# Kernel tuning notes

Hardware: AMD Instinct MI355X
Metric: run time of the kernel (lower is better)

The kernel has to match this reference:

```python
import jax, jax.numpy as jnp
import numpy as np

HEAD_DIM = 128
NUM_HEADS = 16
GROUP_SIZE = 8


def setup_inputs() -> dict:
    key = jax.random.key(0)
    k1, k2, k3 = jax.random.split(key, 3)
    B, T, K = 2, 2048, 2048
    query = jax.random.normal(k1, (B, T, NUM_HEADS * HEAD_DIM), dtype=jnp.float32)
    k_ = jax.random.normal(k2, (B, K, NUM_HEADS, HEAD_DIM), dtype=jnp.float32)
    v_ = jax.random.normal(k3, (B, K, NUM_HEADS, HEAD_DIM), dtype=jnp.float32)
    return {"query": query, "key": k_, "value": v_}


def reference(query, key, value):
    B, T, _ = query.shape
    g = GROUP_SIZE
    # (B, T//g, g, H, D)
    gq = query.reshape(B, T // g, g, NUM_HEADS, HEAD_DIM)
    scale = jnp.sqrt(jnp.asarray(HEAD_DIM, dtype=query.dtype))
    # scores: (B, T//g, g, H, K)
    scores = jnp.einsum('btghd,bkhd->btghk', gq, key) / scale
    attention = jax.nn.softmax(scores, axis=-1)
    out = jnp.einsum('btghk,bkhd->btghd', attention, value)
    return out.reshape(B, T, -1)
```

## Files before the change

### kernel.cpp

```cpp
#include <hip/hip_runtime.h>


#define T_   2048
#define KLEN 2048
#define H_   16
#define D_   128
#define BH_  32
#define NT_  (KLEN / 64)

typedef unsigned short u16;
typedef short bf16x8 __attribute__((ext_vector_type(8), may_alias));
typedef float f32x4 __attribute__((ext_vector_type(4)));
typedef float f32x8 __attribute__((ext_vector_type(8), may_alias));
typedef float f32x16 __attribute__((ext_vector_type(16)));
typedef unsigned int u32a __attribute__((may_alias));
typedef u16 u16a __attribute__((may_alias));

__device__ __forceinline__ u16 f2bf(float f) {
    unsigned int u = __builtin_bit_cast(unsigned int, f);
    u += 0x7fffu + ((u >> 16) & 1u);
    return (u16)(u >> 16);
}
__device__ __forceinline__ unsigned int pk2(float a, float b) {
    unsigned int r;
    asm("v_cvt_pk_bf16_f32 %0, %1, %2" : "=v"(r) : "v"(a), "v"(b));
    return r;
}
__device__ __forceinline__ void pl_swap(unsigned int& a, unsigned int& b) {
    asm("v_permlane32_swap_b32 %0, %1" : "+v"(a), "+v"(b));
}

__device__ __forceinline__ void async_cp16(const void* g, void* l) {
    __builtin_amdgcn_global_load_lds(
        (const __attribute__((address_space(1))) unsigned int*)g,
        (__attribute__((address_space(3))) unsigned int*)l, 16, 0, 0);
}

#define FR_ELEMS ((size_t)KLEN * D_)
#define WS_NEED  (2 * BH_ * FR_ELEMS * sizeof(u16))
#define SM_BUF   32768

__global__ __launch_bounds__(256)
void prep_fused(const float* __restrict__ k_g, const float* __restrict__ v_g,
                u16* __restrict__ kf, u16* __restrict__ vf) {
    __shared__ __align__(16) unsigned char smk[16384];
    __shared__ __align__(16) unsigned char smv[16384];
    const int kt64 = blockIdx.x & 31;
    const int bh   = blockIdx.x >> 5;
    const int b = bh >> 4, h = bh & 15;
    const int tid = threadIdx.x;

    {
        const float* kbase = k_g + ((size_t)(b * KLEN + kt64 * 64) * H_ + h) * D_;
        #pragma unroll
        for (int i = 0; i < 4; ++i) {
            const int gid  = tid + 256 * i;
            const int row  = gid >> 4;
            const int col8 = gid & 15;
            f32x8 kv = *(const f32x8*)(kbase + (size_t)row * (H_ * D_) + col8 * 8);
            uint4 w;
            w.x = pk2(kv[0], kv[1]); w.y = pk2(kv[2], kv[3]);
            w.z = pk2(kv[4], kv[5]); w.w = pk2(kv[6], kv[7]);
            *(uint4*)(smk + row * 256 + ((col8 ^ (row & 15)) * 16)) = w;
        }
    }
    {
        const float* vbase = v_g + ((size_t)b * KLEN * H_ + h) * D_;
        const int sc0 = tid & 15;
        const int spr = tid >> 4;
        #pragma unroll
        for (int rr = 0; rr < 2; ++rr) {
            const int r0 = 2 * (spr + 16 * rr);
            const float* vp = vbase + (size_t)(kt64 * 64 + r0) * (H_ * D_) + sc0 * 8;
            f32x8 va = *(const f32x8*)vp;
            f32x8 vb = *(const f32x8*)(vp + H_ * D_);
            const int g_hi = r0 >> 3;
            const int woff = (r0 & 7) * 2;
            #pragma unroll
            for (int j = 0; j < 8; ++j) {
                const int d = sc0 * 8 + j;
                const int g = g_hi ^ ((d ^ (d >> 3)) & 7);
                *(u32a*)(smv + d * 128 + g * 16 + woff) = pk2(va[j], vb[j]);
            }
        }
    }
    __syncthreads();
    {
        u16* obase = kf + (size_t)bh * FR_ELEMS + (size_t)kt64 * 8192;
        #pragma unroll
        for (int i = 0; i < 4; ++i) {
            const int gid    = tid + 256 * i;
            const int lane   = gid & 63;
            const int dchunk = (gid >> 6) & 7;
            const int ktile  = gid >> 9;
            const int key  = ktile * 32 + (lane & 31);
            const int col8 = dchunk * 2 + (lane >> 5);
            uint4 w = *(const uint4*)(smk + key * 256 + ((col8 ^ (key & 15)) * 16));
            *(uint4*)(obase + (size_t)gid * 8) = w;
        }
    }
    {
        u16* obase = vf + (size_t)bh * FR_ELEMS;
        #pragma unroll
        for (int i = 0; i < 4; ++i) {
            const int gid   = tid + 256 * i;
            const int lane  = gid & 63;
            const int ntile = (gid >> 6) & 3;
            const int kc    = (gid >> 8) & 3;
            const int key0  = kc * 16 + (lane >> 5) * 8;
            const int d     = ntile * 32 + (lane & 31);
            const int g     = (key0 >> 3) ^ ((d ^ (d >> 3)) & 7);
            uint4 w = *(const uint4*)(smv + d * 128 + g * 16);
            *(uint4*)(obase + ((size_t)(kt64 * 16 + kc * 4 + ntile) * 64 + lane) * 8) = w;
        }
    }
}


struct PA2 { bf16x8 f0, f1; };

__device__ __forceinline__ PA2 softmax_pack(f32x16 st, float kexp, float& lacc) {
    float p[16];
    #pragma unroll
    for (int r = 0; r < 16; ++r) p[r] = exp2f(st[r] * kexp);
    lacc += (((p[0] + p[1]) + (p[2] + p[3])) + ((p[4] + p[5]) + (p[6] + p[7])))
          + (((p[8] + p[9]) + (p[10] + p[11])) + ((p[12] + p[13]) + (p[14] + p[15])));
    unsigned int a0 = pk2(p[0], p[1]),   b0 = pk2(p[4], p[5]);
    unsigned int a1 = pk2(p[2], p[3]),   b1 = pk2(p[6], p[7]);
    unsigned int a2 = pk2(p[8], p[9]),   b2 = pk2(p[12], p[13]);
    unsigned int a3 = pk2(p[10], p[11]), b3 = pk2(p[14], p[15]);
    pl_swap(a0, b0); pl_swap(a1, b1); pl_swap(a2, b2); pl_swap(a3, b3);
    uint4 w0; w0.x = a0; w0.y = a1; w0.z = b0; w0.w = b1;
    uint4 w1; w1.x = a2; w1.y = a3; w1.z = b2; w1.w = b3;
    PA2 r;
    r.f0 = __builtin_bit_cast(bf16x8, w0);
    r.f1 = __builtin_bit_cast(bf16x8, w1);
    return r;
}

__global__ __launch_bounds__(256, 1)
void gqa_fa7(const float* __restrict__ q_g, const u16* __restrict__ kf,
             const u16* __restrict__ vf, float* __restrict__ o_g) {
    __shared__ __align__(16) unsigned char smem[2 * SM_BUF];

    const int lane = threadIdx.x & 63;
    const int wave = threadIdx.x >> 6;
    const int half = lane >> 5;
    const int col  = lane & 31;

    const int blk = blockIdx.x;
    const int bh  = (blk & 7) * 4 + (blk >> 6);
    const int qt  = (blk >> 3) & 7;
    const int b = bh >> 4, h = bh & 15;

    const int q0 = qt * 256 + wave * 64;

    bf16x8 qfA[8], qfB[8];
    {
        const float* qbase = q_g + (size_t)(b * T_ + q0 + col) * (H_ * D_)
                                 + h * D_ + half * 8;
        #pragma unroll
        for (int dchunk = 0; dchunk < 8; ++dchunk) {
            f32x8 qv = *(const f32x8*)(qbase + dchunk * 16);
            uint4 w;
            w.x = pk2(qv[0], qv[1]); w.y = pk2(qv[2], qv[3]);
            w.z = pk2(qv[4], qv[5]); w.w = pk2(qv[6], qv[7]);
            qfA[dchunk] = __builtin_bit_cast(bf16x8, w);
        }
        const float* qbase2 = qbase + (size_t)32 * (H_ * D_);
        #pragma unroll
        for (int dchunk = 0; dchunk < 8; ++dchunk) {
            f32x8 qv = *(const f32x8*)(qbase2 + dchunk * 16);
            uint4 w;
            w.x = pk2(qv[0], qv[1]); w.y = pk2(qv[2], qv[3]);
            w.z = pk2(qv[4], qv[5]); w.w = pk2(qv[6], qv[7]);
            qfB[dchunk] = __builtin_bit_cast(bf16x8, w);
        }
    }

    const u16* KFb = kf + (size_t)bh * FR_ELEMS;
    const u16* VFb = vf + (size_t)bh * FR_ELEMS;

    f32x16 accA[4] = {}, accB[4] = {};
    float l_A = 0.f, l_B = 0.f;

    const float kexp = 0.12751744f;

    auto stage = [&](int buf, int kt) {
        const u16* ksrc = KFb + (size_t)kt * 8192;
        const u16* vsrc = VFb + (size_t)kt * 8192;
        unsigned char* base = smem + buf * SM_BUF;
        #pragma unroll
        for (int j = 0; j < 8; ++j) {
            const int idx = wave * 8 + j;
            if (idx < 16)
                async_cp16(ksrc + idx * 512 + lane * 8, base + idx * 1024);
            else
                async_cp16(vsrc + (idx - 16) * 512 + lane * 8,
                           base + 16384 + (idx - 16) * 1024);
        }
    };

    stage(0, 0);
    __syncthreads();

    for (int kt = 0; kt < NT_; ++kt) {
        const int cur = kt & 1;
        if (kt + 1 < NT_) stage(cur ^ 1, kt + 1);

        const unsigned char* kbuf = smem + cur * SM_BUF;
        const unsigned char* vbuf = kbuf + 16384;

        f32x16 sA0 = {}, sA1 = {}, sB0 = {}, sB1 = {};
        __builtin_amdgcn_s_setprio(1);
        #pragma unroll
        for (int dchunk = 0; dchunk < 8; ++dchunk) {
            bf16x8 kfr0 = *(const bf16x8*)(kbuf + dchunk * 1024 + lane * 16);
            bf16x8 kfr1 = *(const bf16x8*)(kbuf + (8 + dchunk) * 1024 + lane * 16);
            sA0 = __builtin_amdgcn_mfma_f32_32x32x16_bf16(kfr0, qfA[dchunk], sA0, 0, 0, 0);
            sA1 = __builtin_amdgcn_mfma_f32_32x32x16_bf16(kfr1, qfA[dchunk], sA1, 0, 0, 0);
            sB0 = __builtin_amdgcn_mfma_f32_32x32x16_bf16(kfr0, qfB[dchunk], sB0, 0, 0, 0);
            sB1 = __builtin_amdgcn_mfma_f32_32x32x16_bf16(kfr1, qfB[dchunk], sB1, 0, 0, 0);
        }
        __builtin_amdgcn_s_setprio(0);

        PA2 pA01 = softmax_pack(sA0, kexp, l_A);
        PA2 pA23 = softmax_pack(sA1, kexp, l_A);
        PA2 pB01 = softmax_pack(sB0, kexp, l_B);
        PA2 pB23 = softmax_pack(sB1, kexp, l_B);

        __builtin_amdgcn_s_setprio(1);
        #pragma unroll
        for (int kc = 0; kc < 4; ++kc) {
            const bf16x8 pa = (kc == 0) ? pA01.f0 : (kc == 1) ? pA01.f1
                            : (kc == 2) ? pA23.f0 : pA23.f1;
            const bf16x8 pb = (kc == 0) ? pB01.f0 : (kc == 1) ? pB01.f1
                            : (kc == 2) ? pB23.f0 : pB23.f1;
            #pragma unroll
            for (int nt2 = 0; nt2 < 4; ++nt2) {
                bf16x8 vfr = *(const bf16x8*)(vbuf + (kc * 4 + nt2) * 1024 + lane * 16);
                accA[nt2] = __builtin_amdgcn_mfma_f32_32x32x16_bf16(pa, vfr, accA[nt2], 0, 0, 0);
                accB[nt2] = __builtin_amdgcn_mfma_f32_32x32x16_bf16(pb, vfr, accB[nt2], 0, 0, 0);
            }
        }
        __builtin_amdgcn_s_setprio(0);

        __syncthreads();
    }

    const float lA_full = l_A + __shfl_xor(l_A, 32);
    const float lB_full = l_B + __shfl_xor(l_B, 32);
    float* lds_l = (float*)smem;
    if (half == 0) {
        lds_l[wave * 64 + col]      = 1.f / lA_full;
        lds_l[wave * 64 + 32 + col] = 1.f / lB_full;
    }
    __syncthreads();
    #pragma unroll
    for (int r = 0; r < 16; ++r) {
        const int qrow = (r & 3) + 8 * (r >> 2) + 4 * half;
        const float invA = lds_l[wave * 64 + qrow];
        const float invB = lds_l[wave * 64 + 32 + qrow];
        float* opA = o_g + (size_t)(b * T_ + q0 + qrow) * (H_ * D_) + h * D_ + col;
        float* opB = opA + (size_t)32 * (H_ * D_);
        #pragma unroll
        for (int nt2 = 0; nt2 < 4; ++nt2) {
            opA[nt2 * 32] = accA[nt2][r] * invA;
            opB[nt2 * 32] = accB[nt2][r] * invB;
        }
    }
}


#define VT_BYTES 16384
#define KT_BYTES (64 * 136 * 2)
#define PWF_BYTES 2304

__global__ __launch_bounds__(256, 2)
void gqa_fa_v1(const float* __restrict__ q_g, const float* __restrict__ k_g,
               const float* __restrict__ v_g, float* __restrict__ o_g) {
    __shared__ __align__(16) unsigned char smem[VT_BYTES + KT_BYTES + 4 * PWF_BYTES];
    unsigned char* VtB = smem;
    unsigned char* KtB = smem + VT_BYTES;
    const int lane = threadIdx.x & 63;
    const int wave = threadIdx.x >> 6;
    const int c    = lane & 15;
    const int quad = lane >> 4;
    const int qt = blockIdx.x & 31;
    const int bh = blockIdx.x >> 5;
    const int h  = bh & 15;
    const int b  = bh >> 4;
    const int q0 = qt * 64 + wave * 16;
    bf16x8 qf[4];
    {
        const float* qbase = q_g + (size_t)(b * T_ + q0 + c) * (H_ * D_) + h * D_ + quad * 8;
        #pragma unroll
        for (int dc = 0; dc < 4; ++dc) {
            f32x8 qv = *(const f32x8*)(qbase + dc * 32);
            uint4 w;
            w.x = pk2(qv[0], qv[1]); w.y = pk2(qv[2], qv[3]);
            w.z = pk2(qv[4], qv[5]); w.w = pk2(qv[6], qv[7]);
            qf[dc] = __builtin_bit_cast(bf16x8, w);
        }
    }
    f32x4 acc_o[8];
    #pragma unroll
    for (int dt = 0; dt < 8; ++dt) acc_o[dt] = (f32x4){0.f, 0.f, 0.f, 0.f};
    float m_i[4], l_i[4];
    #pragma unroll
    for (int r = 0; r < 4; ++r) { m_i[r] = -1e30f; l_i[r] = 0.f; }
    const float kexp = 0.12751744f;
    unsigned char* Pw = smem + VT_BYTES + KT_BYTES + wave * PWF_BYTES;
    const int sc0 = threadIdx.x & 15;
    const int spr = threadIdx.x >> 4;
    const size_t kvstride = (size_t)(H_ * D_);
    const float* kbase = k_g + ((size_t)b * KLEN * H_ + h) * D_;
    const float* vbase = v_g + ((size_t)b * KLEN * H_ + h) * D_;
    for (int kt = 0; kt < KLEN / 64; ++kt) {
        __syncthreads();
        #pragma unroll
        for (int i = 0; i < 4; ++i) {
            const int id   = threadIdx.x + 256 * i;
            const int row  = id >> 4;
            const int dcol = (id & 15) * 8;
            const float* kp = kbase + (size_t)(kt * 64 + row) * kvstride + dcol;
            f32x8 kv = *(const f32x8*)kp;
            uint4 w;
            w.x = pk2(kv[0], kv[1]); w.y = pk2(kv[2], kv[3]);
            w.z = pk2(kv[4], kv[5]); w.w = pk2(kv[6], kv[7]);
            *(uint4*)(KtB + (row * 136 + dcol) * 2) = w;
        }
        #pragma unroll
        for (int rr = 0; rr < 2; ++rr) {
            const int r0 = 2 * (spr + 16 * rr);
            const float* vp = vbase + (size_t)(kt * 64 + r0) * kvstride + sc0 * 8;
            f32x8 va = *(const f32x8*)vp;
            f32x8 vb = *(const f32x8*)(vp + kvstride);
            const int g_hi = r0 >> 3;
            const int woff = (r0 & 7) * 2;
            #pragma unroll
            for (int j = 0; j < 8; ++j) {
                const int d = sc0 * 8 + j;
                const int g = g_hi ^ ((d ^ (d >> 3)) & 7);
                *(u32a*)(VtB + d * 128 + g * 16 + woff) = pk2(va[j], vb[j]);
            }
        }
        __syncthreads();
        f32x4 s[4];
        #pragma unroll
        for (int nt = 0; nt < 4; ++nt) {
            s[nt] = (f32x4){0.f, 0.f, 0.f, 0.f};
            const u16* kfp = (const u16*)KtB + (nt * 16 + c) * 136 + quad * 8;
            #pragma unroll
            for (int dc = 0; dc < 4; ++dc) {
                bf16x8 kfr = *(const bf16x8*)(kfp + dc * 32);
                s[nt] = __builtin_amdgcn_mfma_f32_16x16x32_bf16(qf[dc], kfr, s[nt], 0, 0, 0);
            }
        }
        #pragma unroll
        for (int r = 0; r < 4; ++r) {
            float v = fmaxf(fmaxf(s[0][r], s[1][r]), fmaxf(s[2][r], s[3][r]));
            v = fmaxf(v, __shfl_xor(v, 1));
            v = fmaxf(v, __shfl_xor(v, 2));
            v = fmaxf(v, __shfl_xor(v, 4));
            v = fmaxf(v, __shfl_xor(v, 8));
            const float mnew  = fmaxf(m_i[r], v);
            const float alpha = exp2f((m_i[r] - mnew) * kexp);
            m_i[r] = mnew;
            l_i[r] *= alpha;
            #pragma unroll
            for (int dt = 0; dt < 8; ++dt) acc_o[dt][r] *= alpha;
            float sum = 0.f;
            #pragma unroll
            for (int nt = 0; nt < 4; ++nt) {
                const float p = exp2f((s[nt][r] - mnew) * kexp);
                sum += p;
                *(u16a*)(Pw + ((quad * 4 + r) * 72 + nt * 16 + c) * 2) = f2bf(p);
            }
            float t = sum;
            t += __shfl_xor(t, 1);
            t += __shfl_xor(t, 2);
            t += __shfl_xor(t, 4);
            t += __shfl_xor(t, 8);
            l_i[r] += t;
        }
        __syncthreads();
        #pragma unroll
        for (int kc = 0; kc < 2; ++kc) {
            bf16x8 pf = *(const bf16x8*)(Pw + (c * 72 + kc * 32 + quad * 8) * 2);
            const int k0 = kc * 32 + quad * 8;
            #pragma unroll
            for (int dt = 0; dt < 8; ++dt) {
                const int d = dt * 16 + c;
                const int g = (k0 >> 3) ^ ((d ^ (d >> 3)) & 7);
                bf16x8 vfr = *(const bf16x8*)(VtB + d * 128 + g * 16);
                acc_o[dt] = __builtin_amdgcn_mfma_f32_16x16x32_bf16(pf, vfr, acc_o[dt], 0, 0, 0);
            }
        }
    }
    #pragma unroll
    for (int r = 0; r < 4; ++r) {
        const float inv = 1.f / l_i[r];
        const int qrow = q0 + quad * 4 + r;
        float* op = o_g + (size_t)(b * T_ + qrow) * (H_ * D_) + h * D_ + c;
        #pragma unroll
        for (int dt = 0; dt < 8; ++dt)
            op[dt * 16] = acc_o[dt][r] * inv;
    }
}

extern "C" void kernel_launch(void* const* d_in, const int* in_sizes, int n_in,
                              void* d_out, int out_size, void* d_ws, size_t ws_size,
                              hipStream_t stream) {
    const float* q = (const float*)d_in[0];
    const float* k = (const float*)d_in[1];
    const float* v = (const float*)d_in[2];
    float* o = (float*)d_out;
    if (ws_size >= WS_NEED) {
        u16* kfb = (u16*)d_ws;
        u16* vfb = kfb + (size_t)BH_ * FR_ELEMS;
        prep_fused<<<dim3(1024), dim3(256), 0, stream>>>(k, v, kfb, vfb);
        gqa_fa7<<<dim3(256), dim3(256), 0, stream>>>(q, kfb, vfb, o);
    } else {
        gqa_fa_v1<<<dim3(1024), dim3(256), 0, stream>>>(q, k, v, o);
    }
}
```

Baseline: 237.9 us.

## Software-pipeline QK of next tile with softmax/PV of previous tile using triple buffering

Restructures the attention main loop so the QK^T MFMAs for tile kt are issued before the softmax and PV MFMAs for tile kt-1. LDS goes from double to triple buffering so the previous tile's V stays resident while the next tile loads. The aim is to overlap exp/softmax VALU work with matrix-core work and hide dependency latency. In exchange, registers held across iterations grow (an extra 64 floats of scores) and LDS use rises, which could cause spills.

```diff
diff --git a/kernel.cpp b/kernel.cpp
--- a/kernel.cpp
+++ b/kernel.cpp
@@ -139,9 +139,9 @@
 }
 
 __global__ __launch_bounds__(256, 1)
-void gqa_fa7(const float* __restrict__ q_g, const u16* __restrict__ kf,
+void gqa_fa9(const float* __restrict__ q_g, const u16* __restrict__ kf,
              const u16* __restrict__ vf, float* __restrict__ o_g) {
-    __shared__ __align__(16) unsigned char smem[2 * SM_BUF];
+    __shared__ __align__(16) unsigned char smem[3 * SM_BUF];
 
     const int lane = threadIdx.x & 63;
     const int wave = threadIdx.x >> 6;
@@ -201,34 +201,27 @@
         }
     };
 
-    stage(0, 0);
-    __syncthreads();
-
-    for (int kt = 0; kt < NT_; ++kt) {
-        const int cur = kt & 1;
-        if (kt + 1 < NT_) stage(cur ^ 1, kt + 1);
-
-        const unsigned char* kbuf = smem + cur * SM_BUF;
-        const unsigned char* vbuf = kbuf + 16384;
-
-        f32x16 sA0 = {}, sA1 = {}, sB0 = {}, sB1 = {};
+    auto qk_fused = [&](const unsigned char* kbuf, f32x16& dA0, f32x16& dA1,
+                        f32x16& dB0, f32x16& dB1) {
         __builtin_amdgcn_s_setprio(1);
         #pragma unroll
         for (int dchunk = 0; dchunk < 8; ++dchunk) {
             bf16x8 kfr0 = *(const bf16x8*)(kbuf + dchunk * 1024 + lane * 16);
             bf16x8 kfr1 = *(const bf16x8*)(kbuf + (8 + dchunk) * 1024 + lane * 16);
-            sA0 = __builtin_amdgcn_mfma_f32_32x32x16_bf16(kfr0, qfA[dchunk], sA0, 0, 0, 0);
-            sA1 = __builtin_amdgcn_mfma_f32_32x32x16_bf16(kfr1, qfA[dchunk], sA1, 0, 0, 0);
-            sB0 = __builtin_amdgcn_mfma_f32_32x32x16_bf16(kfr0, qfB[dchunk], sB0, 0, 0, 0);
-            sB1 = __builtin_amdgcn_mfma_f32_32x32x16_bf16(kfr1, qfB[dchunk], sB1, 0, 0, 0);
+            dA0 = __builtin_amdgcn_mfma_f32_32x32x16_bf16(kfr0, qfA[dchunk], dA0, 0, 0, 0);
+            dA1 = __builtin_amdgcn_mfma_f32_32x32x16_bf16(kfr1, qfA[dchunk], dA1, 0, 0, 0);
+            dB0 = __builtin_amdgcn_mfma_f32_32x32x16_bf16(kfr0, qfB[dchunk], dB0, 0, 0, 0);
+            dB1 = __builtin_amdgcn_mfma_f32_32x32x16_bf16(kfr1, qfB[dchunk], dB1, 0, 0, 0);
         }
         __builtin_amdgcn_s_setprio(0);
-
-        PA2 pA01 = softmax_pack(sA0, kexp, l_A);
-        PA2 pA23 = softmax_pack(sA1, kexp, l_A);
-        PA2 pB01 = softmax_pack(sB0, kexp, l_B);
-        PA2 pB23 = softmax_pack(sB1, kexp, l_B);
-
+    };
+
+    auto smpv_fused = [&](f32x16 tA0, f32x16 tA1, f32x16 tB0, f32x16 tB1,
+                          const unsigned char* vbuf) {
+        PA2 pA01 = softmax_pack(tA0, kexp, l_A);
+        PA2 pA23 = softmax_pack(tA1, kexp, l_A);
+        PA2 pB01 = softmax_pack(tB0, kexp, l_B);
+        PA2 pB23 = softmax_pack(tB1, kexp, l_B);
         __builtin_amdgcn_s_setprio(1);
         #pragma unroll
         for (int kc = 0; kc < 4; ++kc) {
@@ -244,9 +237,30 @@
             }
         }
         __builtin_amdgcn_s_setprio(0);
-
+    };
+
+    stage(0, 0);
+    __syncthreads();
+    stage(1, 1);
+    f32x16 psA0 = {}, psA1 = {}, psB0 = {}, psB1 = {};
+    qk_fused(smem, psA0, psA1, psB0, psB1);
+    __syncthreads();
+
+    int cur = 1, prev = 0;
+    for (int kt = 1; kt < NT_; ++kt) {
+        const int nxt = (cur == 2) ? 0 : cur + 1;
+        if (kt + 1 < NT_) stage(nxt, kt + 1);
+
+        f32x16 nsA0 = {}, nsA1 = {}, nsB0 = {}, nsB1 = {};
+        qk_fused(smem + cur * SM_BUF, nsA0, nsA1, nsB0, nsB1);
+        smpv_fused(psA0, psA1, psB0, psB1, smem + prev * SM_BUF + 16384);
+
+        psA0 = nsA0; psA1 = nsA1;
+        psB0 = nsB0; psB1 = nsB1;
+        prev = cur; cur = nxt;
         __syncthreads();
     }
+    smpv_fused(psA0, psA1, psB0, psB1, smem + prev * SM_BUF + 16384);
 
     const float lA_full = l_A + __shfl_xor(l_A, 32);
     const float lB_full = l_B + __shfl_xor(l_B, 32);
@@ -420,7 +434,7 @@
         u16* kfb = (u16*)d_ws;
         u16* vfb = kfb + (size_t)BH_ * FR_ELEMS;
         prep_fused<<<dim3(1024), dim3(256), 0, stream>>>(k, v, kfb, vfb);
-        gqa_fa7<<<dim3(256), dim3(256), 0, stream>>>(q, kfb, vfb, o);
+        gqa_fa9<<<dim3(256), dim3(256), 0, stream>>>(q, kfb, vfb, o);
     } else {
         gqa_fa_v1<<<dim3(1024), dim3(256), 0, stream>>>(q, k, v, o);
     }
```

Result: no change. 234.3 us (-1.5%).
